# Optimization experiments

Hardware: AMD Instinct MI355X
Metric: run time of the kernel (lower is better)

Reference implementation:

```python
import jax, jax.numpy as jnp
import numpy as np

M, N, E, ES, D = 50000, 20000, 200000, 100000, 256

def _ln(x, g, b, eps=1e-5):
    mu = jnp.mean(x, -1, keepdims=True)
    var = jnp.mean((x - mu) ** 2, -1, keepdims=True)
    return (x - mu) * jax.lax.rsqrt(var + eps) * g + b

def _bn_train(x, g, b, eps=1e-5):
    # BatchNorm1d forward in training mode: batch statistics over rows
    mu = jnp.mean(x, 0)
    var = jnp.mean((x - mu) ** 2, 0)
    return (x - mu) * jax.lax.rsqrt(var + eps) * g + b

def _encoder(x, source, Wq, Wk, Wv, Wm, bm, ln1_g, ln1_b, mw1, mb1, mw2, mb2, ln2_g, ln2_b):
    # LoFTR-style linear-attention cross encoder, nhead=1
    Q = jax.nn.elu(x @ Wq) + 1.0          # [L,D]
    K = jax.nn.elu(source @ Wk) + 1.0     # [S,D]
    V = source @ Wv                        # [S,D]
    KV = K.T @ V                           # [D,D]
    Z = Q @ jnp.sum(K, 0) + 1e-6           # [L]
    msg = (Q @ KV) / Z[:, None]            # [L,D]
    msg = _ln(msg @ Wm + bm, ln1_g, ln1_b)
    y = jnp.concatenate([x, msg], -1)      # [L,2D]
    y = jax.nn.relu(y @ mw1 + mb1) @ mw2 + mb2
    return x + _ln(y, ln2_g, ln2_b)

def setup_inputs() -> dict:
    key = jax.random.key(0)
    ks = jax.random.split(key, 20)
    s = 1.0 / np.sqrt(D)
    s2 = 1.0 / np.sqrt(2 * D)
    inp = {
        'h_nodes': jax.random.normal(ks[0], (M, D), jnp.float32),
        's_u': jax.random.normal(ks[1], (N, D), jnp.float32),
        'g_src': jax.random.randint(ks[2], (E,), 0, M, jnp.int32),
        'g_dst': jax.random.randint(ks[3], (E,), 0, M, jnp.int32),
        's_src': jax.random.randint(ks[4], (ES,), 0, N, jnp.int32),
        's_dst': jax.random.randint(ks[5], (ES,), 0, N, jnp.int32),
        'conv_w': jax.random.normal(ks[6], (1, 2, 3), jnp.float32) * 0.3,
        'conv_b': jnp.zeros((1,), jnp.float32),
        'W2': jax.random.normal(ks[7], (D, D), jnp.float32) * s,
        'b2': jnp.zeros((D,), jnp.float32),
        'W4': jax.random.normal(ks[8], (D, D), jnp.float32) * s,
        'b4': jnp.zeros((D,), jnp.float32),
        'bn_g': jnp.ones((D,), jnp.float32),
        'bn_b': jnp.zeros((D,), jnp.float32),
        'Wq': jax.random.normal(ks[9], (D, D), jnp.float32) * s,
        'Wk': jax.random.normal(ks[10], (D, D), jnp.float32) * s,
        'Wv': jax.random.normal(ks[11], (D, D), jnp.float32) * s,
        'Wm': jax.random.normal(ks[12], (D, D), jnp.float32) * s,
        'bm': jnp.zeros((D,), jnp.float32),
        'ln1_g': jnp.ones((D,), jnp.float32),
        'ln1_b': jnp.zeros((D,), jnp.float32),
        'mw1': jax.random.normal(ks[13], (2 * D, 2 * D), jnp.float32) * s2,
        'mb1': jnp.zeros((2 * D,), jnp.float32),
        'mw2': jax.random.normal(ks[14], (2 * D, D), jnp.float32) * s2,
        'mb2': jnp.zeros((D,), jnp.float32),
        'ln2_g': jnp.ones((D,), jnp.float32),
        'ln2_b': jnp.zeros((D,), jnp.float32),
    }
    return inp

def reference(h_nodes, s_u, g_src, g_dst, s_src, s_dst, conv_w, conv_b, W2, b2, W4, b4,
              bn_g, bn_b, Wq, Wk, Wv, Wm, bm, ln1_g, ln1_b, mw1, mb1, mw2, mb2, ln2_g, ln2_b):
    enc = lambda x, src: _encoder(x, src, Wq, Wk, Wv, Wm, bm, ln1_g, ln1_b,
                                  mw1, mb1, mw2, mb2, ln2_g, ln2_b)
    # --- local edge features: gather src/dst, Conv1d(2->1,k=3,p=1), Linear ---
    src = h_nodes[g_src]                         # [E,D]
    dst = h_nodes[g_dst]                         # [E,D]
    edge_in = jnp.stack([src, dst], 1)           # [E,2,D]
    xp = jnp.pad(edge_in, ((0, 0), (0, 0), (1, 1)))
    conv = conv_b[0]
    for c in range(2):
        for j in range(3):
            conv = conv + conv_w[0, c, j] * xp[:, c, j:j + D]
    lr_e_local = conv @ W2 + b2                  # [E,D]
    # --- CrossTransformer (shared encoder weights across HUR/UVR/UUR) ---
    x = enc(h_nodes[:N], s_u)                    # user refinement [N,D]
    h_n = h_nodes.at[:N].set(x)
    edge = enc(h_n[g_src], h_n[g_dst])           # [E,D]
    social_edge = enc(x[s_src], x[s_dst])        # [ES,D]
    # --- fuse + BN + ReLU (dropout off for deterministic reference) ---
    lr_e = edge @ W4 + b4 + lr_e_local
    lr_e = jax.nn.relu(_bn_train(lr_e, bn_g, bn_b))
    social_edge = _bn_train(social_edge, bn_g, bn_b)
    return (lr_e, social_edge)
```

## Files before the change

kernel.cpp:

```cpp
#include <hip/hip_runtime.h>

static constexpr int Mn  = 50000;
static constexpr int Nn  = 20000;
static constexpr int En  = 200000;
static constexpr int ESn = 100000;

typedef short short8v __attribute__((ext_vector_type(8)));
typedef short short4v __attribute__((ext_vector_type(4)));
typedef float f32x4   __attribute__((ext_vector_type(4)));

__device__ __forceinline__ float b2f(unsigned short h) {
  unsigned int u = ((unsigned int)h) << 16;
  return __builtin_bit_cast(float, u);
}
__device__ __forceinline__ unsigned short f2b(float f) {
  unsigned int u = __builtin_bit_cast(unsigned int, f);
  u = (u + 0x7FFFu + ((u >> 16) & 1u)) >> 16;
  return (unsigned short)u;
}
__device__ __forceinline__ void gld16(const void* g, void* l) {
  __builtin_amdgcn_global_load_lds(
      (const __attribute__((address_space(1))) void*)g,
      (__attribute__((address_space(3))) void*)l, 16, 0, 0);
}

__global__ __launch_bounds__(256) void cvt_b(const float* __restrict__ s,
                                             unsigned short* __restrict__ d, long n) {
  long g  = (long)blockIdx.x*256 + threadIdx.x;
  long st = (long)gridDim.x*256;
  for (; g*8 < n; g += st) {
    const float4 a = *(const float4*)(s + g*8);
    const float4 b = *(const float4*)(s + g*8 + 4);
    short8v o;
    o[0]=(short)f2b(a.x); o[1]=(short)f2b(a.y); o[2]=(short)f2b(a.z); o[3]=(short)f2b(a.w);
    o[4]=(short)f2b(b.x); o[5]=(short)f2b(b.y); o[6]=(short)f2b(b.z); o[7]=(short)f2b(b.w);
    *(short8v*)(d + g*8) = o;
  }
}

__global__ __launch_bounds__(128) void wp_build(const float* __restrict__ W, int K, int N,
    unsigned short* __restrict__ WP, int KKd, int kg0) {
  const int t = threadIdx.x;
  const int kk2 = t >> 6, l = t & 63;
  const int c16 = blockIdx.x, ky = blockIdx.y;
  const int k0 = ky*64 + kk2*32 + (l>>4)*8;
  const int n  = c16*16 + (l&15);
  short8v o;
#pragma unroll
  for (int e=0;e<8;++e) o[e] = (short)f2b(W[(long)(k0+e)*N + n]);
  *(short8v*)(WP + (((long)c16*KKd + kg0 + ky*2+kk2)*64 + l)*8) = o;
}

__global__ __launch_bounds__(256) void kvw_mul(const float* __restrict__ KV,
    const float* __restrict__ Wm, float* __restrict__ KVW) {
  const int a = blockIdx.x;
  const int c = threadIdx.x;
  float s = 0.f;
  for (int b = 0; b < 256; ++b) s += KV[a*256 + b] * Wm[(long)b*256 + c];
  KVW[a*256 + c] = s;
}

__global__ __launch_bounds__(256) void count_idx(const int* __restrict__ idx, int n,
                                                 int* __restrict__ cnt) {
  int i = blockIdx.x*256 + threadIdx.x;
  const int st = gridDim.x*256;
  for (; i < n; i += st) atomicAdd(&cnt[idx[i]], 1);
}

__global__ __launch_bounds__(256,3) void gemm_kv(
    const unsigned short* __restrict__ X, int aoff,
    const unsigned short* __restrict__ WkP, const unsigned short* __restrict__ WvP,
    unsigned short* __restrict__ KbT, unsigned short* __restrict__ VbT,
    float* __restrict__ pS, int ldp, int nrows, const int* __restrict__ cntw)
{
  __shared__ short xb[4][64*64];
  const int t = threadIdx.x;
  const int w = t >> 6, l = t & 63, q = l >> 4, hw = l & 15;
  const int r0 = blockIdx.x << 6;

  {
    const int sr = l >> 3, sc = l & 7;
    const int gcol = ((sc ^ sr) << 3);
#pragma unroll
    for (int j=0;j<2;++j) {
      int lr = r0 + j*32 + w*8 + sr;
      int lrc = lr < nrows ? lr : nrows-1;
      const unsigned short* src = X + (long)(aoff+lrc)*256 + gcol;
#pragma unroll
      for (int ks=0;ks<4;++ks)
        gld16(src + ks*64, &xb[ks][(j*32 + w*8)*64]);
    }
  }
  asm volatile("s_waitcnt vmcnt(0)" ::: "memory");
  __builtin_amdgcn_s_barrier();

#pragma unroll
  for (int pass=0; pass<2; ++pass) {
    const unsigned short* WP = pass ? WvP : WkP;
    unsigned short* O = pass ? VbT : KbT;
    f32x4 acc[4][4];
#pragma unroll
    for (int m=0;m<4;++m)
#pragma unroll
      for (int n=0;n<4;++n) acc[m][n] = (f32x4){0.f,0.f,0.f,0.f};
    short8v bfc[4], bfn[4];
#pragma unroll
    for (int n=0;n<4;++n)
      bfc[n] = *(const short8v*)(WP + (((long)(w*4+n)*8)*64 + l)*8);
#pragma unroll
    for (int st=0; st<8; ++st) {
      if (st < 7) {
#pragma unroll
        for (int n=0;n<4;++n)
          bfn[n] = *(const short8v*)(WP + (((long)(w*4+n)*8 + st+1)*64 + l)*8);
      }
      const int ks = st >> 1;
      const int kc = ((st&1)<<2) + q;
      short8v af[4];
#pragma unroll
      for (int m=0;m<4;++m)
        af[m] = *(const short8v*)&xb[ks][(m*16+hw)*64 + ((kc^(hw&7))<<3)];
      __builtin_amdgcn_s_setprio(1);
#pragma unroll
      for (int m=0;m<4;++m)
#pragma unroll
        for (int n=0;n<4;++n)
          acc[m][n] = __builtin_amdgcn_mfma_f32_16x16x32_bf16(af[m], bfc[n], acc[m][n], 0,0,0);
      __builtin_amdgcn_s_setprio(0);
#pragma unroll
      for (int n=0;n<4;++n) bfc[n] = bfn[n];
    }
    float colsum[4] = {0.f,0.f,0.f,0.f};
#pragma unroll
    for (int m=0;m<4;++m)
#pragma unroll
      for (int n=0;n<4;++n) {
        const int c = w*64 + n*16 + hw;
        short4v o4;
#pragma unroll
        for (int i=0;i<4;++i) {
          const int lr = r0 + m*16 + q*4 + i;
          float v = 0.f;
          if (lr < nrows) {
            v = acc[m][n][i];
            if (pass == 0) {
              v = v > 0.f ? v + 1.f : __expf(v);
              if (cntw) v *= (float)cntw[aoff + lr];
            }
          }
          if (pass == 0) colsum[n] += v;
          o4[i] = (short)f2b(v);
        }
        *(short4v*)(O + (long)c*ldp + r0 + m*16 + q*4) = o4;
      }
    if (pass == 0) {
#pragma unroll
      for (int n=0;n<4;++n) {
        float s = colsum[n];
        s += __shfl_xor(s, 16);
        s += __shfl_xor(s, 32);
        if (q == 0) pS[(long)blockIdx.x*256 + w*64 + n*16 + hw] = s;
      }
    }
  }
}

__global__ __launch_bounds__(256) void ksum_red(const float* __restrict__ pS, int nb,
    float* __restrict__ Ks) {
  __shared__ float ws[4];
  const int c = blockIdx.x;
  const int t = threadIdx.x;
  float s = 0.f;
  for (int b = t; b < nb; b += 256) s += pS[(long)b*256 + c];
#pragma unroll
  for (int off=32; off; off>>=1) s += __shfl_xor(s, off);
  if ((t & 63) == 0) ws[t >> 6] = s;
  __syncthreads();
  if (t == 0) Ks[c] += ws[0] + ws[1] + ws[2] + ws[3];
}

__global__ __launch_bounds__(256,4) void ktv_mfma(
    const unsigned short* __restrict__ KbT, const unsigned short* __restrict__ VbT,
    int ldp, int rpp, float* __restrict__ pKV)
{
  const int t  = threadIdx.x;
  const int w  = t >> 6;
  const int l  = t & 63;
  const int q  = l >> 4;
  const int hw = l & 15;
  const int wa = w >> 1, wb = w & 1;
  const int a0 = blockIdx.x << 7;
  const int b0 = blockIdx.y << 7;
  const int rbeg = blockIdx.z * rpp;
  const int rend = min(ldp, rbeg + rpp);

  f32x4 acc[4][4];
#pragma unroll
  for (int m=0;m<4;++m)
#pragma unroll
    for (int n=0;n<4;++n) acc[m][n] = (f32x4){0.f,0.f,0.f,0.f};

  const unsigned short* ap[4];
  const unsigned short* bp[4];
#pragma unroll
  for (int m=0;m<4;++m) ap[m] = KbT + (long)(a0 + wa*64 + m*16 + hw)*ldp + q*8;
#pragma unroll
  for (int n=0;n<4;++n) bp[n] = VbT + (long)(b0 + wb*64 + n*16 + hw)*ldp + q*8;

#pragma unroll 4
  for (int r = rbeg; r < rend; r += 32) {
    short8v af[4], bf[4];
#pragma unroll
    for (int m=0;m<4;++m) af[m] = *(const short8v*)(ap[m] + r);
#pragma unroll
    for (int n=0;n<4;++n) bf[n] = *(const short8v*)(bp[n] + r);
#pragma unroll
    for (int m=0;m<4;++m)
#pragma unroll
      for (int n=0;n<4;++n)
        acc[m][n] = __builtin_amdgcn_mfma_f32_16x16x32_bf16(af[m], bf[n], acc[m][n], 0,0,0);
  }

  const long base = (long)blockIdx.z * 65536;
#pragma unroll
  for (int m=0;m<4;++m)
#pragma unroll
    for (int i=0;i<4;++i) {
      const int a = a0 + wa*64 + m*16 + q*4 + i;
#pragma unroll
      for (int n=0;n<4;++n) {
        const int b = b0 + wb*64 + n*16 + hw;
        pKV[base + (long)a*256 + b] = acc[m][n][i];
      }
    }
}

__global__ __launch_bounds__(256) void kv_accum(const float* __restrict__ pKV, int P,
                                                float* __restrict__ KV) {
  const int i = blockIdx.x*256 + threadIdx.x;
  float s = 0.f;
  for (int p=0;p<P;++p) s += pKV[(long)p*65536 + i];
  KV[i] += s;
}

template<int OMODE>
__global__ __launch_bounds__(256,2) void encB(
    const unsigned short* __restrict__ X, int aoff,
    const unsigned short* __restrict__ WqP, const unsigned short* __restrict__ KVWP,
    const unsigned short* __restrict__ m1P, const unsigned short* __restrict__ m2P,
    const float* __restrict__ Ksum, const float* __restrict__ bmv,
    const float* __restrict__ l1g, const float* __restrict__ l1b,
    const float* __restrict__ mb1, const float* __restrict__ mb2,
    const float* __restrict__ l2g, const float* __restrict__ l2b,
    void* outv, int dc0, int nrows)
{
  __shared__ short xb[4][64*64];
  __shared__ short qb[4][64*64];
  __shared__ short y1b[64*64];
  __shared__ float2 red[64][4];
  __shared__ float Zl[64];

  const int t = threadIdx.x;
  const int w = t >> 6, l = t & 63, q = l >> 4, hw = l & 15;
  const int wc = w;
  const int r0 = blockIdx.x << 6;
  const int sr = l >> 3, sc = l & 7;
  const int gcol = ((sc ^ sr) << 3);

  {
#pragma unroll
    for (int j=0;j<2;++j) {
      int lr = r0 + j*32 + w*8 + sr;
      int lrc = lr < nrows ? lr : nrows-1;
      const unsigned short* src = X + (long)(aoff+lrc)*256 + gcol;
#pragma unroll
      for (int ks=0;ks<4;++ks)
        gld16(src + ks*64, &xb[ks][(j*32 + w*8)*64]);
    }
  }
  asm volatile("s_waitcnt vmcnt(0)" ::: "memory");
  __builtin_amdgcn_s_barrier();

  f32x4 acc[4][4];

  auto GEMM256 = [&](const short* Asrc, const unsigned short* WP) {
#pragma unroll
    for (int m=0;m<4;++m)
#pragma unroll
      for (int n=0;n<4;++n) acc[m][n] = (f32x4){0.f,0.f,0.f,0.f};
    short8v bfc[4], bfn[4];
#pragma unroll
    for (int n=0;n<4;++n)
      bfc[n] = *(const short8v*)(WP + (((long)(wc*4+n)*8)*64 + l)*8);
#pragma unroll
    for (int st=0; st<8; ++st) {
      if (st < 7) {
#pragma unroll
        for (int n=0;n<4;++n)
          bfn[n] = *(const short8v*)(WP + (((long)(wc*4+n)*8 + st+1)*64 + l)*8);
      }
      const int ks = st >> 1;
      const int kc = ((st&1)<<2) + q;
      short8v af[4];
#pragma unroll
      for (int m=0;m<4;++m)
        af[m] = *(const short8v*)&Asrc[ks*4096 + (m*16+hw)*64 + ((kc^(hw&7))<<3)];
      __builtin_amdgcn_s_setprio(1);
#pragma unroll
      for (int m=0;m<4;++m)
#pragma unroll
        for (int n=0;n<4;++n)
          acc[m][n] = __builtin_amdgcn_mfma_f32_16x16x32_bf16(af[m], bfc[n], acc[m][n], 0,0,0);
      __builtin_amdgcn_s_setprio(0);
#pragma unroll
      for (int n=0;n<4;++n) bfc[n] = bfn[n];
    }
  };

  GEMM256(&xb[0][0], WqP);
  {
    float ksv[4];
#pragma unroll
    for (int n=0;n<4;++n) ksv[n] = Ksum[wc*64+n*16+hw];
#pragma unroll
    for (int m=0;m<4;++m)
#pragma unroll
      for (int n=0;n<4;++n)
#pragma unroll
        for (int i=0;i<4;++i) {
          float v = acc[m][n][i];
          acc[m][n][i] = v > 0.f ? v + 1.f : __expf(v);
        }
#pragma unroll
    for (int m=0;m<4;++m)
#pragma unroll
      for (int i=0;i<4;++i) {
        float z = 0.f;
#pragma unroll
        for (int n=0;n<4;++n) z += acc[m][n][i]*ksv[n];
#pragma unroll
        for (int off=1; off<16; off<<=1) z += __shfl_xor(z, off);
        if (hw==0) red[m*16+q*4+i][wc] = make_float2(z, 0.f);
      }
#pragma unroll
    for (int m=0;m<4;++m)
#pragma unroll
      for (int i=0;i<4;++i) {
        const int row = m*16+q*4+i;
        const int sw = row & 7;
#pragma unroll
        for (int n=0;n<4;++n)
          qb[wc][row*64 + (((n*2+(hw>>3)) ^ sw)<<3) + (hw&7)] = (short)f2b(acc[m][n][i]);
      }
  }
  __syncthreads();
  if (wc==0 && hw==0) {
#pragma unroll
    for (int m=0;m<4;++m)
#pragma unroll
      for (int i=0;i<4;++i) {
        const int row = m*16+q*4+i;
        Zl[row] = red[row][0].x + red[row][1].x + red[row][2].x + red[row][3].x + 1e-6f;
      }
  }

  GEMM256(&qb[0][0], KVWP);
  __syncthreads();
#pragma unroll
  for (int m=0;m<4;++m) {
    const f32x4 z = *(const f32x4*)&Zl[m*16+q*4];
#pragma unroll
    for (int i=0;i<4;++i) {
      const float iz = 1.f / z[i];
#pragma unroll
      for (int n=0;n<4;++n) acc[m][n][i] *= iz;
    }
  }
  {
    float lg[4], lb[4];
#pragma unroll
    for (int n=0;n<4;++n) {
      const int c = wc*64+n*16+hw;
      const float bv = bmv[c];
      lg[n] = l1g[c]; lb[n] = l1b[c];
#pragma unroll
      for (int m=0;m<4;++m)
#pragma unroll
        for (int i=0;i<4;++i) acc[m][n][i] += bv;
    }
    float s1[4][4], s2[4][4];
#pragma unroll
    for (int m=0;m<4;++m)
#pragma unroll
      for (int i=0;i<4;++i) {
        float s=0.f, sq=0.f;
#pragma unroll
        for (int n=0;n<4;++n){ const float v=acc[m][n][i]; s+=v; sq+=v*v; }
        s1[m][i]=s; s2[m][i]=sq;
      }
#pragma unroll
    for (int off=1; off<16; off<<=1)
#pragma unroll
      for (int m=0;m<4;++m)
#pragma unroll
        for (int i=0;i<4;++i) {
          s1[m][i] += __shfl_xor(s1[m][i], off);
          s2[m][i] += __shfl_xor(s2[m][i], off);
        }
    if (hw==0) {
#pragma unroll
      for (int m=0;m<4;++m)
#pragma unroll
        for (int i=0;i<4;++i)
          red[m*16+q*4+i][wc] = make_float2(s1[m][i], s2[m][i]);
    }
    __syncthreads();
#pragma unroll
    for (int m=0;m<4;++m)
#pragma unroll
      for (int i=0;i<4;++i) {
        const int row = m*16+q*4+i;
        float ts=0.f, tq=0.f;
#pragma unroll
        for (int ww=0;ww<4;++ww){ const float2 v=red[row][ww]; ts+=v.x; tq+=v.y; }
        const float mmu = ts*(1.f/256.f);
        float var = tq*(1.f/256.f) - mmu*mmu;
        var = var>0.f ? var : 0.f;
        const float rs = rsqrtf(var + 1e-5f);
        const int sw = row & 7;
#pragma unroll
        for (int n=0;n<4;++n) {
          const float v = (acc[m][n][i]-mmu)*rs*lg[n] + lb[n];
          qb[wc][row*64 + (((n*2+(hw>>3)) ^ sw)<<3) + (hw&7)] = (short)f2b(v);
        }
      }
  }
  __syncthreads();

  f32x4 oacc[4][4];
#pragma unroll
  for (int m=0;m<4;++m)
#pragma unroll
    for (int n=0;n<4;++n) oacc[m][n] = (f32x4){0.f,0.f,0.f,0.f};

  for (int ct=0; ct<8; ++ct) {
    f32x4 ya[4];
#pragma unroll
    for (int m=0;m<4;++m) ya[m] = (f32x4){0.f,0.f,0.f,0.f};
    {
      short8v b0c, b0n;
      b0c = *(const short8v*)(m1P + (((long)(ct*4+wc)*16)*64 + l)*8);
#pragma unroll
      for (int st=0; st<16; ++st) {
        if (st < 15)
          b0n = *(const short8v*)(m1P + (((long)(ct*4+wc)*16 + st+1)*64 + l)*8);
        const int ks = st >> 1;
        const int kc = ((st&1)<<2) + q;
        const short* As_ = (ks<4) ? &xb[ks][0] : &qb[ks-4][0];
        __builtin_amdgcn_s_setprio(1);
#pragma unroll
        for (int m=0;m<4;++m) {
          const short8v af = *(const short8v*)&As_[(m*16+hw)*64 + ((kc^(hw&7))<<3)];
          ya[m] = __builtin_amdgcn_mfma_f32_16x16x32_bf16(af, b0c, ya[m], 0,0,0);
        }
        __builtin_amdgcn_s_setprio(0);
        b0c = b0n;
      }
    }
    const float b1 = mb1[ct*64 + wc*16 + hw];
#pragma unroll
    for (int m=0;m<4;++m)
#pragma unroll
      for (int i=0;i<4;++i) {
        const int row = m*16+q*4+i;
        float v = ya[m][i] + b1; v = v>0.f ? v : 0.f;
        y1b[row*64 + (((wc*2+(hw>>3)) ^ (row&7))<<3) + (hw&7)] = (short)f2b(v);
      }
    __syncthreads();
    {
      short8v bfc[4], bfn[4];
#pragma unroll
      for (int n=0;n<4;++n)
        bfc[n] = *(const short8v*)(m2P + (((long)(wc*4+n)*16 + ct*2)*64 + l)*8);
#pragma unroll
      for (int kk=0;kk<2;++kk) {
        if (kk == 0) {
#pragma unroll
          for (int n=0;n<4;++n)
            bfn[n] = *(const short8v*)(m2P + (((long)(wc*4+n)*16 + ct*2+1)*64 + l)*8);
        }
        const int kc = (kk<<2)+q;
        short8v af[4];
#pragma unroll
        for (int m=0;m<4;++m)
          af[m] = *(const short8v*)&y1b[(m*16+hw)*64 + ((kc^(hw&7))<<3)];
        __builtin_amdgcn_s_setprio(1);
#pragma unroll
        for (int m=0;m<4;++m)
#pragma unroll
          for (int n=0;n<4;++n)
            oacc[m][n] = __builtin_amdgcn_mfma_f32_16x16x32_bf16(af[m], bfc[n], oacc[m][n], 0,0,0);
        __builtin_amdgcn_s_setprio(0);
#pragma unroll
        for (int n=0;n<4;++n) bfc[n] = bfn[n];
      }
    }
    __syncthreads();
  }

  {
    float lg[4], lb[4];
#pragma unroll
    for (int n=0;n<4;++n) {
      const int c = wc*64+n*16+hw;
      const float bv = mb2[c];
      lg[n] = l2g[c]; lb[n] = l2b[c];
#pragma unroll
      for (int m=0;m<4;++m)
#pragma unroll
        for (int i=0;i<4;++i) oacc[m][n][i] += bv;
    }
    float s1[4][4], s2[4][4];
#pragma unroll
    for (int m=0;m<4;++m)
#pragma unroll
      for (int i=0;i<4;++i) {
        float s=0.f, sq=0.f;
#pragma unroll
        for (int n=0;n<4;++n){ const float v=oacc[m][n][i]; s+=v; sq+=v*v; }
        s1[m][i]=s; s2[m][i]=sq;
      }
#pragma unroll
    for (int off=1; off<16; off<<=1)
#pragma unroll
      for (int m=0;m<4;++m)
#pragma unroll
        for (int i=0;i<4;++i) {
          s1[m][i] += __shfl_xor(s1[m][i], off);
          s2[m][i] += __shfl_xor(s2[m][i], off);
        }
    if (hw==0) {
#pragma unroll
      for (int m=0;m<4;++m)
#pragma unroll
        for (int i=0;i<4;++i)
          red[m*16+q*4+i][wc] = make_float2(s1[m][i], s2[m][i]);
    }
    __syncthreads();
#pragma unroll
    for (int m=0;m<4;++m)
#pragma unroll
      for (int i=0;i<4;++i) {
        const int row = m*16+q*4+i;
        const int lr = r0 + row;
        if (lr >= nrows) continue;
        float ts=0.f, tq=0.f;
#pragma unroll
        for (int ww=0;ww<4;++ww){ const float2 v=red[row][ww]; ts+=v.x; tq+=v.y; }
        const float mmu = ts*(1.f/256.f);
        float var = tq*(1.f/256.f) - mmu*mmu;
        var = var>0.f ? var : 0.f;
        const float rs = rsqrtf(var + 1e-5f);
        const int sw = row & 7;
#pragma unroll
        for (int n=0;n<4;++n) {
          const int c = wc*64+n*16+hw;
          float v = (oacc[m][n][i]-mmu)*rs*lg[n] + lb[n];
          v += b2f((unsigned short)xb[wc][row*64 + (((n*2+(hw>>3)) ^ sw)<<3) + (hw&7)]);
          const long off2 = (long)(dc0+lr)*256 + c;
          if constexpr (OMODE == 1) ((float*)outv)[off2] = v;
          else ((unsigned short*)outv)[off2] = f2b(v);
        }
      }
  }
}

__global__ __launch_bounds__(256,3) void node_w4(
    const unsigned short* __restrict__ X, const unsigned short* __restrict__ W4P,
    float* __restrict__ EW4, int nrows)
{
  __shared__ short xb[4][64*64];
  const int t = threadIdx.x;
  const int w = t >> 6, l = t & 63, q = l >> 4, hw = l & 15;
  const int r0 = blockIdx.x << 6;
  {
    const int sr = l >> 3, sc = l & 7;
    const int gcol = ((sc ^ sr) << 3);
#pragma unroll
    for (int j=0;j<2;++j) {
      int lr = r0 + j*32 + w*8 + sr;
      int lrc = lr < nrows ? lr : nrows-1;
      const unsigned short* src = X + (long)lrc*256 + gcol;
#pragma unroll
      for (int ks=0;ks<4;++ks)
        gld16(src + ks*64, &xb[ks][(j*32 + w*8)*64]);
    }
  }
  asm volatile("s_waitcnt vmcnt(0)" ::: "memory");
  __builtin_amdgcn_s_barrier();

  f32x4 acc[4][4];
#pragma unroll
  for (int m=0;m<4;++m)
#pragma unroll
    for (int n=0;n<4;++n) acc[m][n] = (f32x4){0.f,0.f,0.f,0.f};
  short8v bfc[4], bfn[4];
#pragma unroll
  for (int n=0;n<4;++n)
    bfc[n] = *(const short8v*)(W4P + (((long)(w*4+n)*8)*64 + l)*8);
#pragma unroll
  for (int st=0; st<8; ++st) {
    if (st < 7) {
#pragma unroll
      for (int n=0;n<4;++n)
        bfn[n] = *(const short8v*)(W4P + (((long)(w*4+n)*8 + st+1)*64 + l)*8);
    }
    const int ks = st >> 1;
    const int kc = ((st&1)<<2) + q;
    short8v af[4];
#pragma unroll
    for (int m=0;m<4;++m)
      af[m] = *(const short8v*)&xb[ks][(m*16+hw)*64 + ((kc^(hw&7))<<3)];
    __builtin_amdgcn_s_setprio(1);
#pragma unroll
    for (int m=0;m<4;++m)
#pragma unroll
      for (int n=0;n<4;++n)
        acc[m][n] = __builtin_amdgcn_mfma_f32_16x16x32_bf16(af[m], bfc[n], acc[m][n], 0,0,0);
    __builtin_amdgcn_s_setprio(0);
#pragma unroll
    for (int n=0;n<4;++n) bfc[n] = bfn[n];
  }
#pragma unroll
  for (int m=0;m<4;++m)
#pragma unroll
    for (int i=0;i<4;++i) {
      const int lr = r0 + m*16 + q*4 + i;
      if (lr >= nrows) continue;
#pragma unroll
      for (int n=0;n<4;++n)
        EW4[(long)lr*256 + w*64 + n*16 + hw] = acc[m][n][i];
    }
}

__global__ __launch_bounds__(256,3) void edge_final(
    const unsigned short* __restrict__ convB, const unsigned short* __restrict__ W2P,
    const float* __restrict__ EW4, const int* __restrict__ gsrc, int aoff,
    const float* __restrict__ b4, const float* __restrict__ b2,
    float* __restrict__ lr_e, int dc0, int nrows)
{
  __shared__ short xb[4][64*64];
  const int t = threadIdx.x;
  const int w = t >> 6, l = t & 63, q = l >> 4, hw = l & 15;
  const int r0 = blockIdx.x << 6;
  {
    const int sr = l >> 3, sc = l & 7;
    const int gcol = ((sc ^ sr) << 3);
#pragma unroll
    for (int j=0;j<2;++j) {
      int lr = r0 + j*32 + w*8 + sr;
      int lrc = lr < nrows ? lr : nrows-1;
      const unsigned short* src = convB + (long)lrc*256 + gcol;
#pragma unroll
      for (int ks=0;ks<4;++ks)
        gld16(src + ks*64, &xb[ks][(j*32 + w*8)*64]);
    }
  }
  asm volatile("s_waitcnt vmcnt(0)" ::: "memory");
  __builtin_amdgcn_s_barrier();

  f32x4 acc[4][4];
#pragma unroll
  for (int m=0;m<4;++m)
#pragma unroll
    for (int n=0;n<4;++n) acc[m][n] = (f32x4){0.f,0.f,0.f,0.f};
  short8v bfc[4], bfn[4];
#pragma unroll
  for (int n=0;n<4;++n)
    bfc[n] = *(const short8v*)(W2P + (((long)(w*4+n)*8)*64 + l)*8);
#pragma unroll
  for (int st=0; st<8; ++st) {
    if (st < 7) {
#pragma unroll
      for (int n=0;n<4;++n)
        bfn[n] = *(const short8v*)(W2P + (((long)(w*4+n)*8 + st+1)*64 + l)*8);
    }
    const int ks = st >> 1;
    const int kc = ((st&1)<<2) + q;
    short8v af[4];
#pragma unroll
    for (int m=0;m<4;++m)
      af[m] = *(const short8v*)&xb[ks][(m*16+hw)*64 + ((kc^(hw&7))<<3)];
    __builtin_amdgcn_s_setprio(1);
#pragma unroll
    for (int m=0;m<4;++m)
#pragma unroll
      for (int n=0;n<4;++n)
        acc[m][n] = __builtin_amdgcn_mfma_f32_16x16x32_bf16(af[m], bfc[n], acc[m][n], 0,0,0);
    __builtin_amdgcn_s_setprio(0);
#pragma unroll
    for (int n=0;n<4;++n) bfc[n] = bfn[n];
  }
  float bia[4];
#pragma unroll
  for (int n=0;n<4;++n) {
    const int c = w*64+n*16+hw;
    bia[n] = b4[c] + b2[c];
  }
#pragma unroll
  for (int m=0;m<4;++m)
#pragma unroll
    for (int i=0;i<4;++i) {
      const int lr = r0 + m*16 + q*4 + i;
      if (lr >= nrows) continue;
      const long rid = (long)gsrc[aoff + lr];
#pragma unroll
      for (int n=0;n<4;++n) {
        const int c = w*64+n*16+hw;
        lr_e[(long)(dc0+lr)*256 + c] = acc[m][n][i] + EW4[rid*256 + c] + bia[n];
      }
    }
}

__global__ __launch_bounds__(256) void conv_rows(const float* __restrict__ h,
    const int* __restrict__ gs, const int* __restrict__ gd, int gr0, int rows,
    const float* __restrict__ cw, const float* __restrict__ cb,
    unsigned short* __restrict__ Cc) {
  const int w = threadIdx.x >> 6, l = threadIdx.x & 63;
  const int r = blockIdx.x*4 + w;
  if (r >= rows) return;
  const float4 s = *(const float4*)(h + (long)gs[gr0+r]*256 + l*4);
  const float4 d = *(const float4*)(h + (long)gd[gr0+r]*256 + l*4);
  float smw = __shfl_up(s.w, 1); if (l==0) smw = 0.f;
  float spx = __shfl_down(s.x, 1); if (l==63) spx = 0.f;
  float dmw = __shfl_up(d.w, 1); if (l==0) dmw = 0.f;
  float dpx = __shfl_down(d.x, 1); if (l==63) dpx = 0.f;
  const float c0=cw[0],c1=cw[1],c2=cw[2],c3=cw[3],c4=cw[4],c5=cw[5],b=cb[0];
  const float o0 = b + c0*smw + c1*s.x + c2*s.y + c3*dmw + c4*d.x + c5*d.y;
  const float o1 = b + c0*s.x + c1*s.y + c2*s.z + c3*d.x + c4*d.y + c5*d.z;
  const float o2 = b + c0*s.y + c1*s.z + c2*s.w + c3*d.y + c4*d.z + c5*d.w;
  const float o3 = b + c0*s.z + c1*s.w + c2*spx + c3*d.z + c4*d.w + c5*dpx;
  short4v o;
  o[0]=(short)f2b(o0); o[1]=(short)f2b(o1); o[2]=(short)f2b(o2); o[3]=(short)f2b(o3);
  *(short4v*)(Cc + (long)r*256 + l*4) = o;
}

__global__ __launch_bounds__(256) void bn_stats(const float* __restrict__ X, long rows,
    int rpb, float* __restrict__ part) {
  const int p = blockIdx.x, w = threadIdx.x>>6, l = threadIdx.x&63;
  long r = (long)p*rpb + w;
  long r1 = (long)(p+1)*rpb; if (r1 > rows) r1 = rows;
  f32x4 s = (f32x4){0,0,0,0}, s2 = (f32x4){0,0,0,0};
  for (; r < r1; r += 4) {
    const float4 v = *(const float4*)(X + r*256 + l*4);
    s[0]+=v.x; s[1]+=v.y; s[2]+=v.z; s[3]+=v.w;
    s2[0]+=v.x*v.x; s2[1]+=v.y*v.y; s2[2]+=v.z*v.z; s2[3]+=v.w*v.w;
  }
  const long pe = (long)p*4 + w;
  *(f32x4*)&part[pe*512 + l*4] = s;
  *(f32x4*)&part[pe*512 + 256 + l*4] = s2;
}

__global__ __launch_bounds__(256) void bnw_stats(const float* __restrict__ X,
    const int* __restrict__ cnt, int rows, float* __restrict__ part) {
  const int b = blockIdx.x, c = threadIdx.x;
  float s=0.f, s2=0.f;
  for (int r=b; r<rows; r+=64) {
    const float wgt = (float)cnt[r];
    if (wgt != 0.f) {
      const float v = X[(long)r*256 + c];
      s += wgt*v; s2 += wgt*v*v;
    }
  }
  part[(long)b*512 + c] = s;
  part[(long)b*512 + 256 + c] = s2;
}

__global__ __launch_bounds__(256) void bn_mid(const float* __restrict__ part, int PE,
    float* __restrict__ mid) {
  const int g = blockIdx.x, c = threadIdx.x;
  float s=0.f, s2=0.f;
  for (int p=g; p<PE; p+=64) {
    s  += part[(long)p*512 + c];
    s2 += part[(long)p*512 + 256 + c];
  }
  mid[(long)g*512 + c] = s;
  mid[(long)g*512 + 256 + c] = s2;
}

__global__ __launch_bounds__(256) void bn_finalize(const float* __restrict__ part, int P,
    long rows, const float* __restrict__ g, const float* __restrict__ b,
    float* __restrict__ scale, float* __restrict__ shift) {
  const int c = threadIdx.x;
  float s=0.f, s2=0.f;
  for (int p=0;p<P;++p) { s += part[(long)p*512 + c]; s2 += part[(long)p*512 + 256 + c]; }
  const float inv = 1.f/(float)rows;
  const float mu = s*inv;
  float var = s2*inv - mu*mu;
  var = var > 0.f ? var : 0.f;
  const float rs = rsqrtf(var + 1e-5f);
  scale[c] = g[c]*rs;
  shift[c] = b[c] - mu*g[c]*rs;
}

template<bool R>
__global__ __launch_bounds__(256) void bn_apply(float* __restrict__ X, long rows,
    const float* __restrict__ sc, const float* __restrict__ sh) {
  const long n4 = rows*64;
  long i = (long)blockIdx.x*256 + threadIdx.x;
  const long st = (long)gridDim.x*256;
  for (; i<n4; i+=st) {
    const int cq = (int)(i & 63);
    float4 v = ((float4*)X)[i];
    const float4 s4 = ((const float4*)sc)[cq];
    const float4 h4 = ((const float4*)sh)[cq];
    v.x = v.x*s4.x + h4.x; v.y = v.y*s4.y + h4.y;
    v.z = v.z*s4.z + h4.z; v.w = v.w*s4.w + h4.w;
    if (R) { v.x=fmaxf(v.x,0.f); v.y=fmaxf(v.y,0.f); v.z=fmaxf(v.z,0.f); v.w=fmaxf(v.w,0.f); }
    ((float4*)X)[i] = v;
  }
}

__global__ __launch_bounds__(256) void bn_apply_gather(const float* __restrict__ nodeS,
    const int* __restrict__ sidx, long rows,
    const float* __restrict__ sc, const float* __restrict__ sh,
    float* __restrict__ out) {
  const long n4 = rows*64;
  long i = (long)blockIdx.x*256 + threadIdx.x;
  const long st = (long)gridDim.x*256;
  for (; i<n4; i+=st) {
    const long row = i >> 6;
    const int cq = (int)(i & 63);
    const long rid = (long)sidx[row];
    float4 v = *(const float4*)(nodeS + rid*256 + cq*4);
    const float4 s4 = ((const float4*)sc)[cq];
    const float4 h4 = ((const float4*)sh)[cq];
    v.x = v.x*s4.x + h4.x; v.y = v.y*s4.y + h4.y;
    v.z = v.z*s4.z + h4.z; v.w = v.w*s4.w + h4.w;
    ((float4*)out)[i] = v;
  }
}

struct Ctx {
  const unsigned short *WkP,*WvP,*WqP,*m1P,*m2P;
  unsigned short* KVWP;
  const float *Wm;
  float* KVW;
  const float *bm,*l1g,*l1b,*mb1,*mb2,*l2g,*l2b;
  unsigned short *bufA,*bufB;
  float *pKV,*pS,*KV;
  long CH;
  hipStream_t st;
};

static void phaseA(const Ctx& c, long S, const unsigned short* Bsrc, const int* cnt) {
  hipMemsetAsync(c.KV, 0, 65792*sizeof(float), c.st);
  for (long s0=0; s0<S; s0+=c.CH) {
    const int n = (int)((S-s0 < c.CH) ? (S-s0) : c.CH);
    const int gb = (n+63)/64;
    const int ldp = gb*64;
    gemm_kv<<<gb,256,0,c.st>>>(Bsrc, (int)s0, c.WkP, c.WvP, c.bufA, c.bufB, c.pS, ldp, n, cnt);
    const int P = (ldp+511)/512;
    ktv_mfma<<<dim3(2,2,P),256,0,c.st>>>(c.bufA, c.bufB, ldp, 512, c.pKV);
    kv_accum<<<256,256,0,c.st>>>(c.pKV, P, c.KV);
    ksum_red<<<256,256,0,c.st>>>(c.pS, gb, c.KV+65536);
  }
  kvw_mul<<<256,256,0,c.st>>>(c.KV, c.Wm, c.KVW);
  wp_build<<<dim3(16,4),128,0,c.st>>>(c.KVW, 256, 256, c.KVWP, 8, 0);
}

template<int OMODE>
static void phaseB(const Ctx& c, long L, const unsigned short* Asrc, void* out) {
  const float* Ksum = c.KV + 65536;
  for (long l0=0; l0<L; l0+=c.CH) {
    const int n = (int)((L-l0 < c.CH) ? (L-l0) : c.CH);
    const int gb = (n+63)/64;
    encB<OMODE><<<gb,256,0,c.st>>>(Asrc, (int)l0,
        c.WqP, c.KVWP, c.m1P, c.m2P, Ksum, c.bm, c.l1g, c.l1b,
        c.mb1, c.mb2, c.l2g, c.l2b, out, (int)l0, n);
  }
}

extern "C" void kernel_launch(void* const* d_in, const int* in_sizes, int n_in,
                              void* d_out, int out_size, void* d_ws, size_t ws_size,
                              hipStream_t stream) {
  const float* h_nodes = (const float*)d_in[0];
  const float* s_u     = (const float*)d_in[1];
  const int*   g_src   = (const int*)d_in[2];
  const int*   g_dst   = (const int*)d_in[3];
  const int*   s_src   = (const int*)d_in[4];
  const int*   s_dst   = (const int*)d_in[5];
  const float* conv_w  = (const float*)d_in[6];
  const float* conv_b  = (const float*)d_in[7];
  const float* W2      = (const float*)d_in[8];
  const float* b2      = (const float*)d_in[9];
  const float* W4      = (const float*)d_in[10];
  const float* b4      = (const float*)d_in[11];
  const float* bn_g    = (const float*)d_in[12];
  const float* bn_b    = (const float*)d_in[13];
  const float* Wq      = (const float*)d_in[14];
  const float* Wk      = (const float*)d_in[15];
  const float* Wv      = (const float*)d_in[16];
  const float* Wm      = (const float*)d_in[17];
  const float* bm      = (const float*)d_in[18];
  const float* l1g     = (const float*)d_in[19];
  const float* l1b     = (const float*)d_in[20];
  const float* mw1     = (const float*)d_in[21];
  const float* mb1     = (const float*)d_in[22];
  const float* mw2     = (const float*)d_in[23];
  const float* mb2     = (const float*)d_in[24];
  const float* l2g     = (const float*)d_in[25];
  const float* l2b     = (const float*)d_in[26];
  (void)in_sizes; (void)n_in; (void)out_size;

  float* lr_e = (float*)d_out;
  float* soc  = lr_e + (size_t)En*256;

  char* base = (char*)d_ws;
  size_t off = 0;
  auto carve = [&](size_t bytes)->void* {
    void* p = (void*)(base + off);
    off = (off + bytes + 255) & ~(size_t)255;
    return p;
  };
  unsigned short* h_nb = (unsigned short*)carve((size_t)Mn*256*2);
  unsigned short* s_ub = (unsigned short*)carve((size_t)Nn*256*2);
  unsigned short* WkP  = (unsigned short*)carve(65536*2);
  unsigned short* WvP  = (unsigned short*)carve(65536*2);
  unsigned short* WqP  = (unsigned short*)carve(65536*2);
  unsigned short* m1P  = (unsigned short*)carve(262144*2);
  unsigned short* m2P  = (unsigned short*)carve(131072*2);
  unsigned short* W4P  = (unsigned short*)carve(65536*2);
  unsigned short* W2P  = (unsigned short*)carve(65536*2);
  unsigned short* KVWP = (unsigned short*)carve(65536*2);
  float* KV            = (float*)carve(65792*4);
  float* KVW           = (float*)carve(65536*4);
  float* bnpart        = (float*)carve((size_t)2048*512*4);
  float* bnmid         = (float*)carve((size_t)64*512*4);
  float* bnscale       = (float*)carve(256*4);
  float* bnshift       = (float*)carve(256*4);
  unsigned short* nodeE= (unsigned short*)carve((size_t)Mn*256*2);
  float* EW4           = (float*)carve((size_t)Mn*256*4);
  float* nodeS         = (float*)carve((size_t)Nn*256*4);
  int* cntg            = (int*)carve((size_t)Mn*4);
  int* cnts            = (int*)carve((size_t)Nn*4);
  int* cntss           = (int*)carve((size_t)Nn*4);

  const size_t remain = ws_size > off ? ws_size - off : 0;
  long CH = (long)(remain / 1589248) * 1024;
  if (CH > 65536) CH = 65536;
  if (CH < 2048)  CH = 2048;
  unsigned short* bufA = (unsigned short*)carve((size_t)CH*256*2);
  unsigned short* bufB = (unsigned short*)carve((size_t)CH*256*2);
  float* pKV           = (float*)carve((size_t)((CH+511)/512)*65536*4);
  float* pS            = (float*)carve((size_t)(CH/64)*256*4);

  cvt_b<<<2048,256,0,stream>>>(h_nodes, h_nb, (long)Mn*256);
  cvt_b<<<1024,256,0,stream>>>(s_u, s_ub, (long)Nn*256);
  wp_build<<<dim3(16,4),128,0,stream>>>(Wk, 256,256, WkP, 8, 0);
  wp_build<<<dim3(16,4),128,0,stream>>>(Wv, 256,256, WvP, 8, 0);
  wp_build<<<dim3(16,4),128,0,stream>>>(Wq, 256,256, WqP, 8, 0);
  wp_build<<<dim3(32,8),128,0,stream>>>(mw1, 512,512, m1P, 16, 0);
  wp_build<<<dim3(16,8),128,0,stream>>>(mw2, 512,256, m2P, 16, 0);
  wp_build<<<dim3(16,4),128,0,stream>>>(W4, 256,256, W4P, 8, 0);
  wp_build<<<dim3(16,4),128,0,stream>>>(W2, 256,256, W2P, 8, 0);
  hipMemsetAsync(cntg, 0, (size_t)Mn*4, stream);
  hipMemsetAsync(cnts, 0, (size_t)Nn*4, stream);
  hipMemsetAsync(cntss,0, (size_t)Nn*4, stream);
  count_idx<<<512,256,0,stream>>>(g_dst, En, cntg);
  count_idx<<<512,256,0,stream>>>(s_dst, ESn, cnts);
  count_idx<<<512,256,0,stream>>>(s_src, ESn, cntss);

  Ctx c;
  c.WkP=WkP; c.WvP=WvP; c.WqP=WqP; c.m1P=m1P; c.m2P=m2P;
  c.KVWP=KVWP; c.Wm=Wm; c.KVW=KVW;
  c.bm=bm; c.l1g=l1g; c.l1b=l1b; c.mb1=mb1; c.mb2=mb2; c.l2g=l2g; c.l2b=l2b;
  c.bufA=bufA; c.bufB=bufB;
  c.pKV=pKV; c.pS=pS; c.KV=KV;
  c.CH=CH; c.st=stream;

  phaseA(c, Nn, s_ub, nullptr);
  phaseB<0>(c, Nn, h_nb, h_nb);

  phaseA(c, Mn, h_nb, cntg);
  phaseB<0>(c, Mn, h_nb, nodeE);
  node_w4<<<(Mn+63)/64,256,0,stream>>>(nodeE, W4P, EW4, Mn);
  for (long e0=0; e0<En; e0+=CH) {
    const int n = (int)(((long)En-e0 < CH) ? (En-e0) : CH);
    conv_rows<<<(n+3)/4,256,0,stream>>>(h_nodes, g_src, g_dst, (int)e0, n, conv_w, conv_b, bufA);
    edge_final<<<(n+63)/64,256,0,stream>>>(bufA, W2P, EW4, g_src, (int)e0, b4, b2,
                                           lr_e, (int)e0, n);
  }

  phaseA(c, Nn, h_nb, cnts);
  phaseB<1>(c, Nn, h_nb, nodeS);
  bnw_stats<<<64,256,0,stream>>>(nodeS, cntss, Nn, bnmid);
  bn_finalize<<<1,256,0,stream>>>(bnmid, 64, (long)ESn, bn_g, bn_b, bnscale, bnshift);
  bn_apply_gather<<<2048,256,0,stream>>>(nodeS, s_src, (long)ESn, bnscale, bnshift, soc);

  {
    const int P3 = (En+511)/512;
    bn_stats<<<P3,256,0,stream>>>(lr_e,(long)En,512,bnpart);
    bn_mid<<<64,256,0,stream>>>(bnpart, P3*4, bnmid);
    bn_finalize<<<1,256,0,stream>>>(bnmid,64,(long)En,bn_g,bn_b,bnscale,bnshift);
    bn_apply<true><<<2048,256,0,stream>>>(lr_e,(long)En,bnscale,bnshift);
  }
}
```

Before: 1.264 ms.

## Fuse W4 projection into encoder epilogue and conv gather into edge GEMM

The encoder output for all nodes is now staged in shared memory and multiplied by W4 inside the encoder kernel (new OMODE 2), which removes the separate node_w4 kernel and the bf16 nodeE round trip through global memory. The Conv1d edge feature computation is folded into edge_final: each block gathers src/dst rows, convolves them and writes bf16 straight into swizzled LDS before the W2 GEMM. This drops the conv_rows kernel, the bufA intermediate and the chunked launch loop. In exchange the encoder epilogue does more work and holds more registers, and the gather inside edge_final is serialized per wave.

```diff
diff --git a/kernel.cpp b/kernel.cpp
--- a/kernel.cpp
+++ b/kernel.cpp
@@ -252,6 +252,7 @@
     const float* __restrict__ l1g, const float* __restrict__ l1b,
     const float* __restrict__ mb1, const float* __restrict__ mb2,
     const float* __restrict__ l2g, const float* __restrict__ l2b,
+    const unsigned short* __restrict__ WfP,
     void* outv, int dc0, int nrows)
 {
   __shared__ short xb[4][64*64];
@@ -567,37 +568,66 @@
           const int c = wc*64+n*16+hw;
           float v = (oacc[m][n][i]-mmu)*rs*lg[n] + lb[n];
           v += b2f((unsigned short)xb[wc][row*64 + (((n*2+(hw>>3)) ^ sw)<<3) + (hw&7)]);
-          const long off2 = (long)(dc0+lr)*256 + c;
-          if constexpr (OMODE == 1) ((float*)outv)[off2] = v;
-          else ((unsigned short*)outv)[off2] = f2b(v);
+          if constexpr (OMODE == 2) {
+            qb[wc][row*64 + (((n*2+(hw>>3)) ^ sw)<<3) + (hw&7)] = (short)f2b(v);
+          } else {
+            const long off2 = (long)(dc0+lr)*256 + c;
+            if constexpr (OMODE == 1) ((float*)outv)[off2] = v;
+            else ((unsigned short*)outv)[off2] = f2b(v);
+          }
         }
       }
   }
-}
-
-__global__ __launch_bounds__(256,3) void node_w4(
-    const unsigned short* __restrict__ X, const unsigned short* __restrict__ W4P,
-    float* __restrict__ EW4, int nrows)
+
+  if constexpr (OMODE == 2) {
+    __syncthreads();
+    GEMM256(&qb[0][0], WfP);
+#pragma unroll
+    for (int m=0;m<4;++m)
+#pragma unroll
+      for (int i=0;i<4;++i) {
+        const int lr = r0 + m*16 + q*4 + i;
+        if (lr >= nrows) continue;
+#pragma unroll
+        for (int n=0;n<4;++n)
+          ((float*)outv)[(long)(dc0+lr)*256 + wc*64+n*16+hw] = acc[m][n][i];
+      }
+  }
+}
+
+__global__ __launch_bounds__(256,3) void edge_final(
+    const float* __restrict__ h, const int* __restrict__ gs, const int* __restrict__ gd,
+    const float* __restrict__ cw, const float* __restrict__ cb,
+    const unsigned short* __restrict__ W2P, const float* __restrict__ EW4,
+    const float* __restrict__ b4, const float* __restrict__ b2,
+    float* __restrict__ lr_e, int nrows)
 {
   __shared__ short xb[4][64*64];
   const int t = threadIdx.x;
   const int w = t >> 6, l = t & 63, q = l >> 4, hw = l & 15;
   const int r0 = blockIdx.x << 6;
-  {
-    const int sr = l >> 3, sc = l & 7;
-    const int gcol = ((sc ^ sr) << 3);
-#pragma unroll
-    for (int j=0;j<2;++j) {
-      int lr = r0 + j*32 + w*8 + sr;
-      int lrc = lr < nrows ? lr : nrows-1;
-      const unsigned short* src = X + (long)lrc*256 + gcol;
-#pragma unroll
-      for (int ks=0;ks<4;++ks)
-        gld16(src + ks*64, &xb[ks][(j*32 + w*8)*64]);
-    }
-  }
-  asm volatile("s_waitcnt vmcnt(0)" ::: "memory");
-  __builtin_amdgcn_s_barrier();
+
+  const float c0=cw[0],c1=cw[1],c2=cw[2],c3=cw[3],c4=cw[4],c5=cw[5],cbb=cb[0];
+  for (int it=0; it<16; ++it) {
+    const int row = w*16 + it;
+    const int lr = r0 + row;
+    const int lrc = lr < nrows ? lr : nrows-1;
+    const float4 s = *(const float4*)(h + (long)gs[lrc]*256 + l*4);
+    const float4 d = *(const float4*)(h + (long)gd[lrc]*256 + l*4);
+    float smw = __shfl_up(s.w, 1); if (l==0) smw = 0.f;
+    float spx = __shfl_down(s.x, 1); if (l==63) spx = 0.f;
+    float dmw = __shfl_up(d.w, 1); if (l==0) dmw = 0.f;
+    float dpx = __shfl_down(d.x, 1); if (l==63) dpx = 0.f;
+    short4v o;
+    o[0]=(short)f2b(cbb + c0*smw + c1*s.x + c2*s.y + c3*dmw + c4*d.x + c5*d.y);
+    o[1]=(short)f2b(cbb + c0*s.x + c1*s.y + c2*s.z + c3*d.x + c4*d.y + c5*d.z);
+    o[2]=(short)f2b(cbb + c0*s.y + c1*s.z + c2*s.w + c3*d.y + c4*d.z + c5*d.w);
+    o[3]=(short)f2b(cbb + c0*s.z + c1*s.w + c2*spx + c3*d.z + c4*d.w + c5*dpx);
+    const int ks = l >> 4;
+    const int g  = (l & 15) >> 1;
+    *(short4v*)&xb[ks][row*64 + ((g ^ (row&7))<<3) + (l&1)*4] = o;
+  }
+  __syncthreads();
 
   f32x4 acc[4][4];
 #pragma unroll
@@ -607,13 +637,13 @@
   short8v bfc[4], bfn[4];
 #pragma unroll
   for (int n=0;n<4;++n)
-    bfc[n] = *(const short8v*)(W4P + (((long)(w*4+n)*8)*64 + l)*8);
+    bfc[n] = *(const short8v*)(W2P + (((long)(w*4+n)*8)*64 + l)*8);
 #pragma unroll
   for (int st=0; st<8; ++st) {
     if (st < 7) {
 #pragma unroll
       for (int n=0;n<4;++n)
-        bfn[n] = *(const short8v*)(W4P + (((long)(w*4+n)*8 + st+1)*64 + l)*8);
+        bfn[n] = *(const short8v*)(W2P + (((long)(w*4+n)*8 + st+1)*64 + l)*8);
     }
     const int ks = st >> 1;
     const int kc = ((st&1)<<2) + q;
@@ -631,118 +661,25 @@
 #pragma unroll
     for (int n=0;n<4;++n) bfc[n] = bfn[n];
   }
+  float bia[4];
+#pragma unroll
+  for (int n=0;n<4;++n) {
+    const int c = w*64+n*16+hw;
+    bia[n] = b4[c] + b2[c];
+  }
 #pragma unroll
   for (int m=0;m<4;++m)
 #pragma unroll
     for (int i=0;i<4;++i) {
       const int lr = r0 + m*16 + q*4 + i;
       if (lr >= nrows) continue;
-#pragma unroll
-      for (int n=0;n<4;++n)
-        EW4[(long)lr*256 + w*64 + n*16 + hw] = acc[m][n][i];
-    }
-}
-
-__global__ __launch_bounds__(256,3) void edge_final(
-    const unsigned short* __restrict__ convB, const unsigned short* __restrict__ W2P,
-    const float* __restrict__ EW4, const int* __restrict__ gsrc, int aoff,
-    const float* __restrict__ b4, const float* __restrict__ b2,
-    float* __restrict__ lr_e, int dc0, int nrows)
-{
-  __shared__ short xb[4][64*64];
-  const int t = threadIdx.x;
-  const int w = t >> 6, l = t & 63, q = l >> 4, hw = l & 15;
-  const int r0 = blockIdx.x << 6;
-  {
-    const int sr = l >> 3, sc = l & 7;
-    const int gcol = ((sc ^ sr) << 3);
-#pragma unroll
-    for (int j=0;j<2;++j) {
-      int lr = r0 + j*32 + w*8 + sr;
-      int lrc = lr < nrows ? lr : nrows-1;
-      const unsigned short* src = convB + (long)lrc*256 + gcol;
-#pragma unroll
-      for (int ks=0;ks<4;++ks)
-        gld16(src + ks*64, &xb[ks][(j*32 + w*8)*64]);
-    }
-  }
-  asm volatile("s_waitcnt vmcnt(0)" ::: "memory");
-  __builtin_amdgcn_s_barrier();
-
-  f32x4 acc[4][4];
-#pragma unroll
-  for (int m=0;m<4;++m)
-#pragma unroll
-    for (int n=0;n<4;++n) acc[m][n] = (f32x4){0.f,0.f,0.f,0.f};
-  short8v bfc[4], bfn[4];
-#pragma unroll
-  for (int n=0;n<4;++n)
-    bfc[n] = *(const short8v*)(W2P + (((long)(w*4+n)*8)*64 + l)*8);
-#pragma unroll
-  for (int st=0; st<8; ++st) {
-    if (st < 7) {
-#pragma unroll
-      for (int n=0;n<4;++n)
-        bfn[n] = *(const short8v*)(W2P + (((long)(w*4+n)*8 + st+1)*64 + l)*8);
-    }
-    const int ks = st >> 1;
-    const int kc = ((st&1)<<2) + q;
-    short8v af[4];
-#pragma unroll
-    for (int m=0;m<4;++m)
-      af[m] = *(const short8v*)&xb[ks][(m*16+hw)*64 + ((kc^(hw&7))<<3)];
-    __builtin_amdgcn_s_setprio(1);
-#pragma unroll
-    for (int m=0;m<4;++m)
-#pragma unroll
-      for (int n=0;n<4;++n)
-        acc[m][n] = __builtin_amdgcn_mfma_f32_16x16x32_bf16(af[m], bfc[n], acc[m][n], 0,0,0);
-    __builtin_amdgcn_s_setprio(0);
-#pragma unroll
-    for (int n=0;n<4;++n) bfc[n] = bfn[n];
-  }
-  float bia[4];
-#pragma unroll
-  for (int n=0;n<4;++n) {
-    const int c = w*64+n*16+hw;
-    bia[n] = b4[c] + b2[c];
-  }
-#pragma unroll
-  for (int m=0;m<4;++m)
-#pragma unroll
-    for (int i=0;i<4;++i) {
-      const int lr = r0 + m*16 + q*4 + i;
-      if (lr >= nrows) continue;
-      const long rid = (long)gsrc[aoff + lr];
+      const long rid = (long)gs[lr];
 #pragma unroll
       for (int n=0;n<4;++n) {
         const int c = w*64+n*16+hw;
-        lr_e[(long)(dc0+lr)*256 + c] = acc[m][n][i] + EW4[rid*256 + c] + bia[n];
-      }
-    }
-}
-
-__global__ __launch_bounds__(256) void conv_rows(const float* __restrict__ h,
-    const int* __restrict__ gs, const int* __restrict__ gd, int gr0, int rows,
-    const float* __restrict__ cw, const float* __restrict__ cb,
-    unsigned short* __restrict__ Cc) {
-  const int w = threadIdx.x >> 6, l = threadIdx.x & 63;
-  const int r = blockIdx.x*4 + w;
-  if (r >= rows) return;
-  const float4 s = *(const float4*)(h + (long)gs[gr0+r]*256 + l*4);
-  const float4 d = *(const float4*)(h + (long)gd[gr0+r]*256 + l*4);
-  float smw = __shfl_up(s.w, 1); if (l==0) smw = 0.f;
-  float spx = __shfl_down(s.x, 1); if (l==63) spx = 0.f;
-  float dmw = __shfl_up(d.w, 1); if (l==0) dmw = 0.f;
-  float dpx = __shfl_down(d.x, 1); if (l==63) dpx = 0.f;
-  const float c0=cw[0],c1=cw[1],c2=cw[2],c3=cw[3],c4=cw[4],c5=cw[5],b=cb[0];
-  const float o0 = b + c0*smw + c1*s.x + c2*s.y + c3*dmw + c4*d.x + c5*d.y;
-  const float o1 = b + c0*s.x + c1*s.y + c2*s.z + c3*d.x + c4*d.y + c5*d.z;
-  const float o2 = b + c0*s.y + c1*s.z + c2*s.w + c3*d.y + c4*d.z + c5*d.w;
-  const float o3 = b + c0*s.z + c1*s.w + c2*spx + c3*d.z + c4*d.w + c5*dpx;
-  short4v o;
-  o[0]=(short)f2b(o0); o[1]=(short)f2b(o1); o[2]=(short)f2b(o2); o[3]=(short)f2b(o3);
-  *(short4v*)(Cc + (long)r*256 + l*4) = o;
+        lr_e[(long)lr*256 + c] = acc[m][n][i] + EW4[rid*256 + c] + bia[n];
+      }
+    }
 }
 
 __global__ __launch_bounds__(256) void bn_stats(const float* __restrict__ X, long rows,
@@ -870,14 +807,15 @@
 }
 
 template<int OMODE>
-static void phaseB(const Ctx& c, long L, const unsigned short* Asrc, void* out) {
+static void phaseB(const Ctx& c, long L, const unsigned short* Asrc, void* out,
+                   const unsigned short* WfP) {
   const float* Ksum = c.KV + 65536;
   for (long l0=0; l0<L; l0+=c.CH) {
     const int n = (int)((L-l0 < c.CH) ? (L-l0) : c.CH);
     const int gb = (n+63)/64;
     encB<OMODE><<<gb,256,0,c.st>>>(Asrc, (int)l0,
         c.WqP, c.KVWP, c.m1P, c.m2P, Ksum, c.bm, c.l1g, c.l1b,
-        c.mb1, c.mb2, c.l2g, c.l2b, out, (int)l0, n);
+        c.mb1, c.mb2, c.l2g, c.l2b, WfP, out, (int)l0, n);
   }
 }
 
@@ -939,7 +877,6 @@
   float* bnmid         = (float*)carve((size_t)64*512*4);
   float* bnscale       = (float*)carve(256*4);
   float* bnshift       = (float*)carve(256*4);
-  unsigned short* nodeE= (unsigned short*)carve((size_t)Mn*256*2);
   float* EW4           = (float*)carve((size_t)Mn*256*4);
   float* nodeS         = (float*)carve((size_t)Nn*256*4);
   int* cntg            = (int*)carve((size_t)Mn*4);
@@ -980,20 +917,15 @@
   c.CH=CH; c.st=stream;
 
   phaseA(c, Nn, s_ub, nullptr);
-  phaseB<0>(c, Nn, h_nb, h_nb);
+  phaseB<0>(c, Nn, h_nb, h_nb, nullptr);
 
   phaseA(c, Mn, h_nb, cntg);
-  phaseB<0>(c, Mn, h_nb, nodeE);
-  node_w4<<<(Mn+63)/64,256,0,stream>>>(nodeE, W4P, EW4, Mn);
-  for (long e0=0; e0<En; e0+=CH) {
-    const int n = (int)(((long)En-e0 < CH) ? (En-e0) : CH);
-    conv_rows<<<(n+3)/4,256,0,stream>>>(h_nodes, g_src, g_dst, (int)e0, n, conv_w, conv_b, bufA);
-    edge_final<<<(n+63)/64,256,0,stream>>>(bufA, W2P, EW4, g_src, (int)e0, b4, b2,
-                                           lr_e, (int)e0, n);
-  }
+  phaseB<2>(c, Mn, h_nb, EW4, W4P);
+  edge_final<<<(En+63)/64,256,0,stream>>>(h_nodes, g_src, g_dst, conv_w, conv_b,
+                                          W2P, EW4, b4, b2, lr_e, En);
 
   phaseA(c, Nn, h_nb, cnts);
-  phaseB<1>(c, Nn, h_nb, nodeS);
+  phaseB<1>(c, Nn, h_nb, nodeS, nullptr);
   bnw_stats<<<64,256,0,stream>>>(nodeS, cntss, Nn, bnmid);
   bn_finalize<<<1,256,0,stream>>>(bnmid, 64, (long)ESn, bn_g, bn_b, bnscale, bnshift);
   bn_apply_gather<<<2048,256,0,stream>>>(nodeS, s_src, (long)ESn, bnscale, bnshift, soc);
```

Result: faster. 1.207 ms (-4.5%).
